# Kernel tuning notes

Measured on AMD Instinct MI355X. Metric: run time of the kernel, lower is better.

## Reference

```python
import jax, jax.numpy as jnp
import numpy as np

BATCH, N_REC, D_HIDDEN = 8192, 1024, 2048
RMIN, RMAX = 0.4, 0.99

def _half_glorot(key, shape):
    # VarianceScaling(scale=1/2, fan_avg, uniform): limit = sqrt(3*scale/fan_avg)
    fan_avg = (shape[0] + shape[1]) / 2.0
    limit = np.sqrt(1.5 / fan_avg)
    return jax.random.uniform(key, shape, jnp.float32, -limit, limit)

def setup_inputs() -> dict:
    key = jax.random.key(0)
    ks = jax.random.split(key, 11)
    inputs = jax.random.normal(ks[0], (BATCH, N_REC), jnp.float32)
    state_re = jax.random.normal(ks[1], (BATCH, D_HIDDEN), jnp.float32)
    state_im = jax.random.normal(ks[2], (BATCH, D_HIDDEN), jnp.float32)
    C_re = _half_glorot(ks[3], (D_HIDDEN, N_REC))
    C_im = _half_glorot(ks[4], (D_HIDDEN, N_REC))
    B_re = _half_glorot(ks[5], (N_REC, D_HIDDEN))
    B_im = _half_glorot(ks[6], (N_REC, D_HIDDEN))
    D = jax.random.normal(ks[7], (N_REC,), jnp.float32)
    numax = float(np.log(-np.log(RMIN)))
    numin = float(np.log(-np.log(RMAX)))
    nu = jax.random.uniform(ks[8], (D_HIDDEN,), jnp.float32, numin, numax)
    theta = jax.random.uniform(ks[9], (D_HIDDEN,), jnp.float32, 0.0, 3.14 / 10)
    # gamma initialized to sqrt(1 - |lambda|^2), |lambda| = exp(-exp(nu))
    gamma = jnp.sqrt(1.0 - jnp.exp(-2.0 * jnp.exp(nu)))
    return {"inputs": inputs, "state_re": state_re, "state_im": state_im,
            "B_re": B_re, "B_im": B_im, "C_re": C_re, "C_im": C_im,
            "D": D, "nu": nu, "theta": theta, "gamma": gamma}

def reference(inputs, state_re, state_im, B_re, B_im, C_re, C_im, D, nu, theta, gamma):
    # lambda = exp(-exp(nu) + i*theta), diagonal complex recurrence
    lam = (jnp.exp(-jnp.exp(nu)) * jnp.exp(1j * theta)).astype(jnp.complex64)  # [H]
    x = (state_re + 1j * state_im).astype(jnp.complex64)  # [B,H]
    B = (B_re + 1j * B_im).astype(jnp.complex64)          # [N,H]
    C = (C_re + 1j * C_im).astype(jnp.complex64)          # [H,N]
    u_ = inputs.astype(jnp.complex64)
    new_u = gamma.astype(jnp.complex64) * (u_ @ B)        # [B,H]
    x_ = x * lam + new_u                                  # diag matmul == elementwise
    y = jnp.real(x_ @ C) + D * inputs                     # [B,N]
    return y, jnp.real(x_), jnp.imag(x_)
```

## Files before the change

kernel.cpp:

```cpp
#include <hip/hip_runtime.h>
#include <hip/hip_bf16.h>

typedef __bf16 bf16;
typedef __attribute__((ext_vector_type(8))) __bf16 bf16x8;
typedef __attribute__((ext_vector_type(4))) float floatx4;

#define BATCH 8192
#define NREC  1024
#define DHID  2048

#define GLOBAL_AS __attribute__((address_space(1)))
#define LDS_AS    __attribute__((address_space(3)))

__device__ __forceinline__ bf16 to_bf16(float f) { return (bf16)f; }

__device__ __forceinline__ void async16(const void* g, void* l) {
  __builtin_amdgcn_global_load_lds((const GLOBAL_AS unsigned int*)g,
                                   (LDS_AS unsigned int*)l, 16, 0, 0);
}

__device__ __forceinline__ bf16x8 ldsFrag(const bf16* buf, int row, int q) {
  const int s = (q ^ ((row >> 1) & 3)) * 8;
  return *reinterpret_cast<const bf16x8*>(&buf[row * 32 + s]);
}

__global__ __launch_bounds__(256) void prep_kernel(
    const float* __restrict__ inputs, bf16* __restrict__ A1,
    const float* __restrict__ B_re, const float* __restrict__ B_im,
    bf16* __restrict__ BreT, bf16* __restrict__ BimT,
    const float* __restrict__ C_re, const float* __restrict__ C_im,
    bf16* __restrict__ CcatT,
    const float* __restrict__ nu, const float* __restrict__ theta,
    float* __restrict__ lamRe, float* __restrict__ lamIm)
{
  __shared__ float tile[32][33];
  const int b   = blockIdx.x;
  const int tid = threadIdx.x;

  if (b < 8192) {
    const int idx = b * 256 + tid;
    float4 v = reinterpret_cast<const float4*>(inputs)[idx];
    ushort4 pk;
    pk.x = __builtin_bit_cast(unsigned short, to_bf16(v.x));
    pk.y = __builtin_bit_cast(unsigned short, to_bf16(v.y));
    pk.z = __builtin_bit_cast(unsigned short, to_bf16(v.z));
    pk.w = __builtin_bit_cast(unsigned short, to_bf16(v.w));
    *reinterpret_cast<ushort4*>(A1 + (size_t)idx * 4) = pk;
    return;
  }
  if (b < 16384) {
    const float* src; bf16* dst; int C, dstStride; float scale; int t;
    if (b < 10240)      { t = b - 8192;  src = B_re; dst = BreT;         C = 2048; dstStride = 1024; scale =  1.0f; }
    else if (b < 12288) { t = b - 10240; src = B_im; dst = BimT;         C = 2048; dstStride = 1024; scale =  1.0f; }
    else if (b < 14336) { t = b - 12288; src = C_re; dst = CcatT;        C = 1024; dstStride = 4096; scale =  1.0f; }
    else                { t = b - 14336; src = C_im; dst = CcatT + 2048; C = 1024; dstStride = 4096; scale = -1.0f; }
    const int gx = C / 32;
    const int bx = t % gx, by = t / gx;
    const int c0 = bx * 32, r0 = by * 32;
    const int tx = tid & 31, ty = tid >> 5;
    #pragma unroll
    for (int i = 0; i < 32; i += 8) {
      tile[ty + i][tx] = src[(size_t)(r0 + ty + i) * C + c0 + tx];
    }
    __syncthreads();
    #pragma unroll
    for (int i = 0; i < 32; i += 8) {
      const int c = c0 + ty + i;
      dst[(size_t)c * dstStride + r0 + tx] = to_bf16(scale * tile[tx][ty + i]);
    }
    return;
  }
  const int h = (b - 16384) * 256 + tid;
  if (h < DHID) {
    float tt = expf(-expf(nu[h]));
    lamRe[h] = tt * cosf(theta[h]);
    lamIm[h] = tt * sinf(theta[h]);
  }
}


__global__ __launch_bounds__(512, 3) void gemm1_kernel(
    const bf16* __restrict__ A,
    const bf16* __restrict__ BreT,
    const bf16* __restrict__ BimT,
    const float* __restrict__ state_re,
    const float* __restrict__ state_im,
    const float* __restrict__ gamma,
    const float* __restrict__ lamRe,
    const float* __restrict__ lamIm,
    float* __restrict__ xre_out,
    float* __restrict__ xim_out,
    bf16* __restrict__ Xcat)
{
  __shared__ __align__(16) bf16 Alds[2][128 * 32];
  __shared__ __align__(16) bf16 BreLds[2][128 * 32];
  __shared__ __align__(16) bf16 BimLds[2][128 * 32];

  const int tid = threadIdx.x;
  const int d       = blockIdx.x + blockIdx.y * gridDim.x;
  const int cpx     = (gridDim.x * gridDim.y) >> 3;
  const int logical = (d & 7) * cpx + (d >> 3);
  const int mBase = (logical / gridDim.x) * 128;
  const int hBase = (logical % gridDim.x) * 128;

  const int lane  = tid & 63;
  const int wave  = tid >> 6;
  const int wr    = (wave >> 2) * 64;
  const int wc    = (wave & 3) * 32;
  const int m16   = lane & 15;
  const int q     = lane >> 4;

  floatx4 zero = {0.f, 0.f, 0.f, 0.f};
  floatx4 accRe[4][2], accIm[4][2];
  #pragma unroll
  for (int i = 0; i < 4; ++i)
    #pragma unroll
    for (int j = 0; j < 2; ++j) { accRe[i][j] = zero; accIm[i][j] = zero; }

  const int row0 = tid >> 2;
  const int ss   = ((tid & 3) ^ ((row0 >> 1) & 3)) * 8;
  const int wbase = wave * 512;

  auto stage = [&](int buf, int kt) {
    const size_t aoff = (size_t)(mBase + row0) * 1024 + kt + ss;
    const size_t boff = (size_t)(hBase + row0) * 1024 + kt + ss;
    async16(&A[aoff],    &Alds[buf][wbase]);
    async16(&BreT[boff], &BreLds[buf][wbase]);
    async16(&BimT[boff], &BimLds[buf][wbase]);
  };

  auto computeTile = [&](int buf) {
    bf16x8 aF[4], brF[2], biF[2];
    #pragma unroll
    for (int i = 0; i < 4; ++i)
      aF[i] = ldsFrag(Alds[buf], wr + i * 16 + m16, q);
    #pragma unroll
    for (int j = 0; j < 2; ++j) {
      brF[j] = ldsFrag(BreLds[buf], wc + j * 16 + m16, q);
      biF[j] = ldsFrag(BimLds[buf], wc + j * 16 + m16, q);
    }
    #pragma unroll
    for (int i = 0; i < 4; ++i)
      #pragma unroll
      for (int j = 0; j < 2; ++j) {
        accRe[i][j] = __builtin_amdgcn_mfma_f32_16x16x32_bf16(aF[i], brF[j], accRe[i][j], 0, 0, 0);
        accIm[i][j] = __builtin_amdgcn_mfma_f32_16x16x32_bf16(aF[i], biF[j], accIm[i][j], 0, 0, 0);
      }
  };

  stage(0, 0);
  __syncthreads();
  int cur = 0;
  for (int kt = 32; kt < 1024; kt += 32) {
    stage(cur ^ 1, kt);
    computeTile(cur);
    __syncthreads();
    cur ^= 1;
  }
  computeTile(cur);

  #pragma unroll
  for (int j = 0; j < 2; ++j) {
    const int h  = hBase + wc + j * 16 + m16;
    const float g  = gamma[h];
    const float lr = lamRe[h];
    const float li = lamIm[h];
    #pragma unroll
    for (int i = 0; i < 4; ++i) {
      #pragma unroll
      for (int r = 0; r < 4; ++r) {
        const int row = mBase + wr + i * 16 + q * 4 + r;
        const size_t off = (size_t)row * DHID + h;
        const float ur = g * accRe[i][j][r];
        const float ui = g * accIm[i][j][r];
        const float sr = state_re[off];
        const float si = state_im[off];
        const float xr = sr * lr - si * li + ur;
        const float xi = sr * li + si * lr + ui;
        xre_out[off] = xr;
        xim_out[off] = xi;
        const size_t xoff = (size_t)row * (2 * DHID) + h;
        Xcat[xoff]        = to_bf16(xr);
        Xcat[xoff + DHID] = to_bf16(xi);
      }
    }
  }
}


__global__ __launch_bounds__(512, 4) void gemm2_kernel(
    const bf16* __restrict__ Xcat,
    const bf16* __restrict__ CcatT,
    const float* __restrict__ Dvec,
    const float* __restrict__ inputs,
    float* __restrict__ y)
{
  __shared__ __align__(16) bf16 Alds[2][128 * 32];
  __shared__ __align__(16) bf16 Blds[2][128 * 32];

  const int tid = threadIdx.x;
  const int d       = blockIdx.x + blockIdx.y * gridDim.x;
  const int cpx     = (gridDim.x * gridDim.y) >> 3;
  const int logical = (d & 7) * cpx + (d >> 3);
  const int mBase = (logical / gridDim.x) * 128;
  const int nBase = (logical % gridDim.x) * 128;

  const int lane  = tid & 63;
  const int wave  = tid >> 6;
  const int wr    = (wave >> 2) * 64;
  const int wc    = (wave & 3) * 32;
  const int m16   = lane & 15;
  const int q     = lane >> 4;

  floatx4 zero = {0.f, 0.f, 0.f, 0.f};
  floatx4 acc[4][2];
  #pragma unroll
  for (int i = 0; i < 4; ++i)
    #pragma unroll
    for (int j = 0; j < 2; ++j) acc[i][j] = zero;

  const int row0 = tid >> 2;
  const int ss   = ((tid & 3) ^ ((row0 >> 1) & 3)) * 8;
  const int wbase = wave * 512;

  auto stage = [&](int buf, int kt) {
    const size_t aoff = (size_t)(mBase + row0) * 4096 + kt + ss;
    const size_t boff = (size_t)(nBase + row0) * 4096 + kt + ss;
    async16(&Xcat[aoff],  &Alds[buf][wbase]);
    async16(&CcatT[boff], &Blds[buf][wbase]);
  };

  auto computeTile = [&](int buf) {
    bf16x8 aF[4], bF[2];
    #pragma unroll
    for (int i = 0; i < 4; ++i)
      aF[i] = ldsFrag(Alds[buf], wr + i * 16 + m16, q);
    #pragma unroll
    for (int j = 0; j < 2; ++j)
      bF[j] = ldsFrag(Blds[buf], wc + j * 16 + m16, q);
    #pragma unroll
    for (int i = 0; i < 4; ++i)
      #pragma unroll
      for (int j = 0; j < 2; ++j)
        acc[i][j] = __builtin_amdgcn_mfma_f32_16x16x32_bf16(aF[i], bF[j], acc[i][j], 0, 0, 0);
  };

  stage(0, 0);
  __syncthreads();
  int cur = 0;
  for (int kt = 32; kt < 4096; kt += 32) {
    stage(cur ^ 1, kt);
    computeTile(cur);
    __syncthreads();
    cur ^= 1;
  }
  computeTile(cur);

  #pragma unroll
  for (int j = 0; j < 2; ++j) {
    const int n = nBase + wc + j * 16 + m16;
    const float dv = Dvec[n];
    #pragma unroll
    for (int i = 0; i < 4; ++i) {
      #pragma unroll
      for (int r = 0; r < 4; ++r) {
        const int row = mBase + wr + i * 16 + q * 4 + r;
        const size_t idx = (size_t)row * NREC + n;
        y[idx] = acc[i][j][r] + dv * inputs[idx];
      }
    }
  }
}


extern "C" void kernel_launch(void* const* d_in, const int* in_sizes, int n_in,
                              void* d_out, int out_size, void* d_ws, size_t ws_size,
                              hipStream_t stream) {
  (void)in_sizes; (void)n_in; (void)out_size; (void)ws_size;

  const float* inputs   = (const float*)d_in[0];
  const float* state_re = (const float*)d_in[1];
  const float* state_im = (const float*)d_in[2];
  const float* B_re     = (const float*)d_in[3];
  const float* B_im     = (const float*)d_in[4];
  const float* C_re     = (const float*)d_in[5];
  const float* C_im     = (const float*)d_in[6];
  const float* Dvec     = (const float*)d_in[7];
  const float* nu       = (const float*)d_in[8];
  const float* theta    = (const float*)d_in[9];
  const float* gamma    = (const float*)d_in[10];

  float* out     = (float*)d_out;
  float* y_out   = out;
  float* xre_out = out + (size_t)BATCH * NREC;
  float* xim_out = xre_out + (size_t)BATCH * DHID;

  char* ws = (char*)d_ws;
  bf16*  A1    = (bf16*)(ws + 0);
  bf16*  BreT  = (bf16*)(ws + 16777216);
  bf16*  BimT  = (bf16*)(ws + 20971520);
  bf16*  CcatT = (bf16*)(ws + 25165824);
  bf16*  Xcat  = (bf16*)(ws + 33554432);
  float* lamRe = (float*)(ws + 100663296);
  float* lamIm = (float*)(ws + 100671488);

  prep_kernel<<<dim3(16392), dim3(256), 0, stream>>>(
      inputs, A1, B_re, B_im, BreT, BimT, C_re, C_im, CcatT,
      nu, theta, lamRe, lamIm);

  gemm1_kernel<<<dim3(DHID / 128, BATCH / 128), dim3(512), 0, stream>>>(
      A1, BreT, BimT, state_re, state_im, gamma, lamRe, lamIm, xre_out, xim_out, Xcat);

  gemm2_kernel<<<dim3(NREC / 128, BATCH / 128), dim3(512), 0, stream>>>(
      Xcat, CcatT, Dvec, inputs, y_out);
}
```

Baseline: 554.7 us.

## Enlarge GEMM tiles to 256x128x64 with ping-pong barrier-scheduled MFMA pipeline

```diff
diff --git a/kernel.cpp b/kernel.cpp
--- a/kernel.cpp
+++ b/kernel.cpp
@@ -19,10 +19,14 @@
                                    (LDS_AS unsigned int*)l, 16, 0, 0);
 }
 
-__device__ __forceinline__ bf16x8 ldsFrag(const bf16* buf, int row, int q) {
-  const int s = (q ^ ((row >> 1) & 3)) * 8;
-  return *reinterpret_cast<const bf16x8*>(&buf[row * 32 + s]);
-}
+#define BAR()                                 \
+  do {                                        \
+    asm volatile("" ::: "memory");            \
+    __builtin_amdgcn_s_barrier();             \
+    asm volatile("" ::: "memory");            \
+  } while (0)
+
+#define VMW(N) asm volatile("s_waitcnt vmcnt(" #N ")" ::: "memory")
 
 __global__ __launch_bounds__(256) void prep_kernel(
     const float* __restrict__ inputs, bf16* __restrict__ A1,
@@ -79,7 +83,62 @@
 }
 
 
-__global__ __launch_bounds__(512, 3) void gemm1_kernel(
+#define G1_RDA(BUF, MH)                                                        \
+  {                                                                            \
+    _Pragma("unroll") for (int f = 0; f < 4; ++f) {                            \
+      _Pragma("unroll") for (int ks = 0; ks < 2; ++ks) {                       \
+        const int row_ = wr + ((MH) * 4 + f) * 16 + m16;                       \
+        aF[f][ks] = *reinterpret_cast<const bf16x8*>(                          \
+            &Al[BUF][row_ * 64 + ((((ks << 2) | q) ^ (row_ & 7)) * 8)]);       \
+      }                                                                        \
+    }                                                                          \
+  }
+
+#define G1_RDBRE(BUF)                                                         \
+  {                                                                            \
+    _Pragma("unroll") for (int g = 0; g < 2; ++g) {                            \
+      _Pragma("unroll") for (int ks = 0; ks < 2; ++ks) {                       \
+        const int row_ = wc + g * 16 + m16;                                    \
+        brF[g][ks] = *reinterpret_cast<const bf16x8*>(                         \
+            &BreL[BUF][row_ * 64 + ((((ks << 2) | q) ^ (row_ & 7)) * 8)]);     \
+      }                                                                        \
+    }                                                                          \
+  }
+
+#define G1_RDBIM(BUF)                                                         \
+  {                                                                            \
+    _Pragma("unroll") for (int g = 0; g < 2; ++g) {                            \
+      _Pragma("unroll") for (int ks = 0; ks < 2; ++ks) {                       \
+        const int row_ = wc + g * 16 + m16;                                    \
+        biF[g][ks] = *reinterpret_cast<const bf16x8*>(                         \
+            &BimL[BUF][row_ * 64 + ((((ks << 2) | q) ^ (row_ & 7)) * 8)]);     \
+      }                                                                        \
+    }                                                                          \
+  }
+
+#define G1_MMARE(MH)                                                           \
+  {                                                                            \
+    __builtin_amdgcn_s_setprio(1);                                             \
+    _Pragma("unroll") for (int f = 0; f < 4; ++f)                              \
+      _Pragma("unroll") for (int g = 0; g < 2; ++g)                            \
+        _Pragma("unroll") for (int ks = 0; ks < 2; ++ks)                       \
+          accRe[(MH) * 4 + f][g] = __builtin_amdgcn_mfma_f32_16x16x32_bf16(    \
+              aF[f][ks], brF[g][ks], accRe[(MH) * 4 + f][g], 0, 0, 0);         \
+    __builtin_amdgcn_s_setprio(0);                                             \
+  }
+
+#define G1_MMAIM(MH)                                                           \
+  {                                                                            \
+    __builtin_amdgcn_s_setprio(1);                                             \
+    _Pragma("unroll") for (int f = 0; f < 4; ++f)                              \
+      _Pragma("unroll") for (int g = 0; g < 2; ++g)                            \
+        _Pragma("unroll") for (int ks = 0; ks < 2; ++ks)                       \
+          accIm[(MH) * 4 + f][g] = __builtin_amdgcn_mfma_f32_16x16x32_bf16(    \
+              aF[f][ks], biF[g][ks], accIm[(MH) * 4 + f][g], 0, 0, 0);         \
+    __builtin_amdgcn_s_setprio(0);                                             \
+  }
+
+__global__ __launch_bounds__(512, 2) void gemm1_kernel(
     const bf16* __restrict__ A,
     const bf16* __restrict__ BreT,
     const bf16* __restrict__ BimT,
@@ -92,87 +151,117 @@
     float* __restrict__ xim_out,
     bf16* __restrict__ Xcat)
 {
-  __shared__ __align__(16) bf16 Alds[2][128 * 32];
-  __shared__ __align__(16) bf16 BreLds[2][128 * 32];
-  __shared__ __align__(16) bf16 BimLds[2][128 * 32];
-
-  const int tid = threadIdx.x;
-  const int d       = blockIdx.x + blockIdx.y * gridDim.x;
-  const int cpx     = (gridDim.x * gridDim.y) >> 3;
-  const int logical = (d & 7) * cpx + (d >> 3);
-  const int mBase = (logical / gridDim.x) * 128;
-  const int hBase = (logical % gridDim.x) * 128;
-
+  __shared__ __align__(16) bf16 Al[2][256 * 64];
+  __shared__ __align__(16) bf16 BreL[2][128 * 64];
+  __shared__ __align__(16) bf16 BimL[2][128 * 64];
+
+  const int tid   = threadIdx.x;
+  const int mBase = blockIdx.y * 256;
+  const int hBase = blockIdx.x * 128;
   const int lane  = tid & 63;
   const int wave  = tid >> 6;
-  const int wr    = (wave >> 2) * 64;
+  const int wr    = (wave >> 2) * 128;
   const int wc    = (wave & 3) * 32;
   const int m16   = lane & 15;
   const int q     = lane >> 4;
 
-  floatx4 zero = {0.f, 0.f, 0.f, 0.f};
-  floatx4 accRe[4][2], accIm[4][2];
+  floatx4 accRe[8][2], accIm[8][2];
   #pragma unroll
-  for (int i = 0; i < 4; ++i)
-    #pragma unroll
-    for (int j = 0; j < 2; ++j) { accRe[i][j] = zero; accIm[i][j] = zero; }
-
-  const int row0 = tid >> 2;
-  const int ss   = ((tid & 3) ^ ((row0 >> 1) & 3)) * 8;
-  const int wbase = wave * 512;
-
-  auto stage = [&](int buf, int kt) {
-    const size_t aoff = (size_t)(mBase + row0) * 1024 + kt + ss;
-    const size_t boff = (size_t)(hBase + row0) * 1024 + kt + ss;
-    async16(&A[aoff],    &Alds[buf][wbase]);
-    async16(&BreT[boff], &BreLds[buf][wbase]);
-    async16(&BimT[boff], &BimLds[buf][wbase]);
+  for (int i = 0; i < 8; ++i)
+    #pragma unroll
+    for (int g = 0; g < 2; ++g) {
+      accRe[i][g] = floatx4{0.f, 0.f, 0.f, 0.f};
+      accIm[i][g] = floatx4{0.f, 0.f, 0.f, 0.f};
+    }
+
+  bf16x8 aF[4][2], brF[2][2], biF[2][2];
+
+  auto stA = [&](int buf_, int kt, int half) {
+    #pragma unroll
+    for (int p = 0; p < 2; ++p) {
+      const int pos = p * 512 + tid;
+      const int r   = pos >> 3;
+      const int ss  = ((pos & 7) ^ (r & 7)) * 8;
+      async16(&A[(size_t)(mBase + half * 128 + r) * 1024 + kt * 64 + ss],
+              &Al[buf_][half * 8192 + p * 4096 + wave * 512]);
+    }
   };
-
-  auto computeTile = [&](int buf) {
-    bf16x8 aF[4], brF[2], biF[2];
-    #pragma unroll
-    for (int i = 0; i < 4; ++i)
-      aF[i] = ldsFrag(Alds[buf], wr + i * 16 + m16, q);
-    #pragma unroll
-    for (int j = 0; j < 2; ++j) {
-      brF[j] = ldsFrag(BreLds[buf], wc + j * 16 + m16, q);
-      biF[j] = ldsFrag(BimLds[buf], wc + j * 16 + m16, q);
-    }
-    #pragma unroll
-    for (int i = 0; i < 4; ++i)
-      #pragma unroll
-      for (int j = 0; j < 2; ++j) {
-        accRe[i][j] = __builtin_amdgcn_mfma_f32_16x16x32_bf16(aF[i], brF[j], accRe[i][j], 0, 0, 0);
-        accIm[i][j] = __builtin_amdgcn_mfma_f32_16x16x32_bf16(aF[i], biF[j], accIm[i][j], 0, 0, 0);
-      }
+  auto stBre = [&](int buf_, int kt) {
+    #pragma unroll
+    for (int p = 0; p < 2; ++p) {
+      const int pos = p * 512 + tid;
+      const int r   = pos >> 3;
+      const int ss  = ((pos & 7) ^ (r & 7)) * 8;
+      async16(&BreT[(size_t)(hBase + r) * 1024 + kt * 64 + ss],
+              &BreL[buf_][p * 4096 + wave * 512]);
+    }
   };
-
-  stage(0, 0);
-  __syncthreads();
-  int cur = 0;
-  for (int kt = 32; kt < 1024; kt += 32) {
-    stage(cur ^ 1, kt);
-    computeTile(cur);
-    __syncthreads();
-    cur ^= 1;
-  }
-  computeTile(cur);
+  auto stBim = [&](int buf_, int kt) {
+    #pragma unroll
+    for (int p = 0; p < 2; ++p) {
+      const int pos = p * 512 + tid;
+      const int r   = pos >> 3;
+      const int ss  = ((pos & 7) ^ (r & 7)) * 8;
+      async16(&BimT[(size_t)(hBase + r) * 1024 + kt * 64 + ss],
+              &BimL[buf_][p * 4096 + wave * 512]);
+    }
+  };
+
+  stA(0, 0, 0); stA(0, 0, 1); stBre(0, 0); stBim(0, 0);
+  stBre(1, 1);  stBim(1, 1);
+  VMW(4);
+  BAR();
+
+  #pragma unroll 1
+  for (int it = 0; it < 7; ++it) {
+    const int t0 = 2 * it;
+    G1_RDA(0, 0); G1_RDBRE(0); stA(1, t0 + 1, 0);
+    BAR(); G1_MMARE(0); BAR();
+    G1_RDBIM(0); stA(1, t0 + 1, 1);
+    BAR(); G1_MMAIM(0); BAR();
+    G1_RDA(0, 1); stBre(0, t0 + 2);
+    BAR(); G1_MMAIM(1); BAR();
+    stBim(0, t0 + 2); VMW(4);
+    BAR(); G1_MMARE(1); BAR();
+    G1_RDA(1, 0); G1_RDBRE(1); stA(0, t0 + 2, 0);
+    BAR(); G1_MMARE(0); BAR();
+    G1_RDBIM(1); stA(0, t0 + 2, 1);
+    BAR(); G1_MMAIM(0); BAR();
+    G1_RDA(1, 1); stBre(1, t0 + 3);
+    BAR(); G1_MMAIM(1); BAR();
+    stBim(1, t0 + 3); VMW(4);
+    BAR(); G1_MMARE(1); BAR();
+  }
+  G1_RDA(0, 0); G1_RDBRE(0); stA(1, 15, 0);
+  BAR(); G1_MMARE(0); BAR();
+  G1_RDBIM(0); stA(1, 15, 1);
+  BAR(); G1_MMAIM(0); BAR();
+  G1_RDA(0, 1);
+  BAR(); G1_MMAIM(1); BAR();
+  VMW(0);
+  BAR(); G1_MMARE(1); BAR();
+  G1_RDA(1, 0); G1_RDBRE(1);
+  BAR(); G1_MMARE(0); BAR();
+  G1_RDBIM(1);
+  BAR(); G1_MMAIM(0); BAR();
+  G1_RDA(1, 1);
+  BAR(); G1_MMAIM(1); BAR();
+  G1_MMARE(1);
 
   #pragma unroll
-  for (int j = 0; j < 2; ++j) {
-    const int h  = hBase + wc + j * 16 + m16;
-    const float g  = gamma[h];
+  for (int g = 0; g < 2; ++g) {
+    const int h  = hBase + wc + g * 16 + m16;
+    const float gm = gamma[h];
     const float lr = lamRe[h];
     const float li = lamIm[h];
     #pragma unroll
-    for (int i = 0; i < 4; ++i) {
+    for (int i = 0; i < 8; ++i) {
       #pragma unroll
       for (int r = 0; r < 4; ++r) {
         const int row = mBase + wr + i * 16 + q * 4 + r;
         const size_t off = (size_t)row * DHID + h;
-        const float ur = g * accRe[i][j][r];
-        const float ui = g * accIm[i][j][r];
+        const float ur = gm * accRe[i][g][r];
+        const float ui = gm * accIm[i][g][r];
         const float sr = state_re[off];
         const float si = state_im[off];
         const float xr = sr * lr - si * li + ur;
@@ -188,85 +277,125 @@
 }
 
 
-__global__ __launch_bounds__(512, 4) void gemm2_kernel(
+#define G2_RDA(BUF, MH)                                                        \
+  {                                                                            \
+    _Pragma("unroll") for (int f = 0; f < 4; ++f) {                            \
+      _Pragma("unroll") for (int ks = 0; ks < 2; ++ks) {                       \
+        const int row_ = wr + ((MH) * 4 + f) * 16 + m16;                       \
+        aF[f][ks] = *reinterpret_cast<const bf16x8*>(                          \
+            &Al[BUF][row_ * 64 + ((((ks << 2) | q) ^ (row_ & 7)) * 8)]);       \
+      }                                                                        \
+    }                                                                          \
+  }
+
+#define G2_RDB(BUF)                                                            \
+  {                                                                            \
+    _Pragma("unroll") for (int g = 0; g < 2; ++g) {                            \
+      _Pragma("unroll") for (int ks = 0; ks < 2; ++ks) {                       \
+        const int row_ = wc + g * 16 + m16;                                    \
+        bF[g][ks] = *reinterpret_cast<const bf16x8*>(                          \
+            &Bl[BUF][row_ * 64 + ((((ks << 2) | q) ^ (row_ & 7)) * 8)]);       \
+      }                                                                        \
+    }                                                                          \
+  }
+
+#define G2_MMA(MH)                                                             \
+  {                                                                            \
+    __builtin_amdgcn_s_setprio(1);                                             \
+    _Pragma("unroll") for (int f = 0; f < 4; ++f)                              \
+      _Pragma("unroll") for (int g = 0; g < 2; ++g)                            \
+        _Pragma("unroll") for (int ks = 0; ks < 2; ++ks)                       \
+          acc[(MH) * 4 + f][g] = __builtin_amdgcn_mfma_f32_16x16x32_bf16(      \
+              aF[f][ks], bF[g][ks], acc[(MH) * 4 + f][g], 0, 0, 0);            \
+    __builtin_amdgcn_s_setprio(0);                                             \
+  }
+
+__global__ __launch_bounds__(512, 2) void gemm2_kernel(
     const bf16* __restrict__ Xcat,
     const bf16* __restrict__ CcatT,
     const float* __restrict__ Dvec,
     const float* __restrict__ inputs,
     float* __restrict__ y)
 {
-  __shared__ __align__(16) bf16 Alds[2][128 * 32];
-  __shared__ __align__(16) bf16 Blds[2][128 * 32];
-
-  const int tid = threadIdx.x;
-  const int d       = blockIdx.x + blockIdx.y * gridDim.x;
-  const int cpx     = (gridDim.x * gridDim.y) >> 3;
-  const int logical = (d & 7) * cpx + (d >> 3);
-  const int mBase = (logical / gridDim.x) * 128;
-  const int nBase = (logical % gridDim.x) * 128;
-
+  __shared__ __align__(16) bf16 Al[2][256 * 64];
+  __shared__ __align__(16) bf16 Bl[2][128 * 64];
+
+  const int tid   = threadIdx.x;
+  const int mBase = blockIdx.y * 256;
+  const int nBase = blockIdx.x * 128;
   const int lane  = tid & 63;
   const int wave  = tid >> 6;
-  const int wr    = (wave >> 2) * 64;
+  const int wr    = (wave >> 2) * 128;
   const int wc    = (wave & 3) * 32;
   const int m16   = lane & 15;
   const int q     = lane >> 4;
 
-  floatx4 zero = {0.f, 0.f, 0.f, 0.f};
-  floatx4 acc[4][2];
+  floatx4 acc[8][2];
   #pragma unroll
-  for (int i = 0; i < 4; ++i)
-    #pragma unroll
-    for (int j = 0; j < 2; ++j) acc[i][j] = zero;
-
-  const int row0 = tid >> 2;
-  const int ss   = ((tid & 3) ^ ((row0 >> 1) & 3)) * 8;
-  const int wbase = wave * 512;
-
-  auto stage = [&](int buf, int kt) {
-    const size_t aoff = (size_t)(mBase + row0) * 4096 + kt + ss;
-    const size_t boff = (size_t)(nBase + row0) * 4096 + kt + ss;
-    async16(&Xcat[aoff],  &Alds[buf][wbase]);
-    async16(&CcatT[boff], &Blds[buf][wbase]);
+  for (int i = 0; i < 8; ++i)
+    #pragma unroll
+    for (int g = 0; g < 2; ++g) acc[i][g] = floatx4{0.f, 0.f, 0.f, 0.f};
+
+  bf16x8 aF[4][2], bF[2][2];
+
+  auto stA = [&](int buf_, int kt, int half) {
+    #pragma unroll
+    for (int p = 0; p < 2; ++p) {
+      const int pos = p * 512 + tid;
+      const int r   = pos >> 3;
+      const int ss  = ((pos & 7) ^ (r & 7)) * 8;
+      async16(&Xcat[(size_t)(mBase + half * 128 + r) * 4096 + kt * 64 + ss],
+              &Al[buf_][half * 8192 + p * 4096 + wave * 512]);
+    }
   };
-
-  auto computeTile = [&](int buf) {
-    bf16x8 aF[4], bF[2];
-    #pragma unroll
-    for (int i = 0; i < 4; ++i)
-      aF[i] = ldsFrag(Alds[buf], wr + i * 16 + m16, q);
-    #pragma unroll
-    for (int j = 0; j < 2; ++j)
-      bF[j] = ldsFrag(Blds[buf], wc + j * 16 + m16, q);
-    #pragma unroll
-    for (int i = 0; i < 4; ++i)
-      #pragma unroll
-      for (int j = 0; j < 2; ++j)
-        acc[i][j] = __builtin_amdgcn_mfma_f32_16x16x32_bf16(aF[i], bF[j], acc[i][j], 0, 0, 0);
+  auto stB = [&](int buf_, int kt) {
+    #pragma unroll
+    for (int p = 0; p < 2; ++p) {
+      const int pos = p * 512 + tid;
+      const int r   = pos >> 3;
+      const int ss  = ((pos & 7) ^ (r & 7)) * 8;
+      async16(&CcatT[(size_t)(nBase + r) * 4096 + kt * 64 + ss],
+              &Bl[buf_][p * 4096 + wave * 512]);
+    }
   };
 
-  stage(0, 0);
-  __syncthreads();
-  int cur = 0;
-  for (int kt = 32; kt < 4096; kt += 32) {
-    stage(cur ^ 1, kt);
-    computeTile(cur);
-    __syncthreads();
-    cur ^= 1;
-  }
-  computeTile(cur);
+  stA(0, 0, 0); stA(0, 0, 1); stB(0, 0);
+  stB(1, 1);
+  VMW(2);
+  BAR();
+
+  #pragma unroll 1
+  for (int it = 0; it < 31; ++it) {
+    const int t0 = 2 * it;
+    G2_RDA(0, 0); G2_RDB(0); stA(1, t0 + 1, 0); stA(1, t0 + 1, 1);
+    BAR(); G2_MMA(0); BAR();
+    G2_RDA(0, 1); stB(0, t0 + 2); VMW(2);
+    BAR(); G2_MMA(1); BAR();
+    G2_RDA(1, 0); G2_RDB(1); stA(0, t0 + 2, 0); stA(0, t0 + 2, 1);
+    BAR(); G2_MMA(0); BAR();
+    G2_RDA(1, 1); stB(1, t0 + 3); VMW(2);
+    BAR(); G2_MMA(1); BAR();
+  }
+  G2_RDA(0, 0); G2_RDB(0); stA(1, 63, 0); stA(1, 63, 1);
+  BAR(); G2_MMA(0); BAR();
+  G2_RDA(0, 1); VMW(0);
+  BAR(); G2_MMA(1); BAR();
+  G2_RDA(1, 0); G2_RDB(1);
+  BAR(); G2_MMA(0); BAR();
+  G2_RDA(1, 1);
+  BAR(); G2_MMA(1);
 
   #pragma unroll
-  for (int j = 0; j < 2; ++j) {
-    const int n = nBase + wc + j * 16 + m16;
+  for (int g = 0; g < 2; ++g) {
+    const int n = nBase + wc + g * 16 + m16;
     const float dv = Dvec[n];
     #pragma unroll
-    for (int i = 0; i < 4; ++i) {
+    for (int i = 0; i < 8; ++i) {
       #pragma unroll
       for (int r = 0; r < 4; ++r) {
         const int row = mBase + wr + i * 16 + q * 4 + r;
         const size_t idx = (size_t)row * NREC + n;
-        y[idx] = acc[i][j][r] + dv * inputs[idx];
+        y[idx] = acc[i][g][r] + dv * inputs[idx];
       }
     }
   }
@@ -308,9 +437,9 @@
       inputs, A1, B_re, B_im, BreT, BimT, C_re, C_im, CcatT,
       nu, theta, lamRe, lamIm);
 
-  gemm1_kernel<<<dim3(DHID / 128, BATCH / 128), dim3(512), 0, stream>>>(
+  gemm1_kernel<<<dim3(DHID / 128, BATCH / 256), dim3(512), 0, stream>>>(
       A1, BreT, BimT, state_re, state_im, gamma, lamRe, lamIm, xre_out, xim_out, Xcat);
 
-  gemm2_kernel<<<dim3(NREC / 128, BATCH / 128), dim3(512), 0, stream>>>(
+  gemm2_kernel<<<dim3(NREC / 128, BATCH / 256), dim3(512), 0, stream>>>(
       Xcat, CcatT, Dvec, inputs, y_out);
 }
```

Result: slower. 604.6 us (+9.0%).
